# Kernel optimization log

Measured on AMD Instinct MI355X. Metric: run time of the kernel, lower is better.

The kernel has to match this reference:

```python
import jax, jax.numpy as jnp
import numpy as np

N, F, M, E = 8192, 256, 128, 131072


def setup_inputs() -> dict:
    key = jax.random.key(0)
    k = jax.random.split(key, 6)
    x = jax.random.normal(k[0], (N, F), dtype=jnp.float32)
    edge_index = jax.random.randint(k[1], (2, E), 0, N, dtype=jnp.int64)
    eps = jax.random.normal(k[2], (N, M), dtype=jnp.float32)
    # small init scale so sigmoid(z_i . z_j) isn't saturated
    W_mu = jax.random.normal(k[3], (F, M), dtype=jnp.float32) * 0.05
    b_mu = jnp.zeros((M,), dtype=jnp.float32)
    W_sig = jax.random.normal(k[4], (F, M), dtype=jnp.float32) * 0.05
    b_sig = jnp.zeros((M,), dtype=jnp.float32)
    return {"x": x, "edge_index": edge_index, "eps": eps,
            "W_mu": W_mu, "b_mu": b_mu, "W_sig": W_sig, "b_sig": b_sig}


def reference(x, edge_index, eps, W_mu, b_mu, W_sig, b_sig):
    # Gaussian encoder: Normal(mu, exp(logstd)), Independent over latent dim
    mu = x @ W_mu + b_mu                      # [N, M]
    logstd = x @ W_sig + b_sig                # [N, M]
    sigma = jnp.exp(logstd)
    z = mu + sigma * eps                      # rsample, [N, M]

    # decoder.probability(dot(z_i, z_j)) = sigmoid(logit); vectorized as Z @ Z.T
    logits = z @ z.T                          # [N, N]

    # symmetric adjacency labels from edge_index (either direction counts)
    src, dst = edge_index[0], edge_index[1]
    adj = jnp.zeros((N, N), dtype=jnp.float32)
    adj = adj.at[src, dst].set(1.0)
    adj = adj.at[dst, src].set(1.0)

    # BCE(sigmoid(s), y) summed over unordered pairs i < j (stable logits form)
    per_pair = jax.nn.softplus(logits) - adj * logits  # = -[y log p + (1-y) log(1-p)]
    triu = jnp.triu(jnp.ones((N, N), dtype=bool), k=1)
    bce = jnp.sum(jnp.where(triu, per_pair, 0.0))

    # sum_i KL( N(mu_i, sigma_i) || N(0, I) )
    kl = jnp.sum(0.5 * (sigma * sigma + mu * mu - 1.0) - logstd)

    return bce + 0.001 * kl
```

## Files before the change

kernel.cpp:

```cpp
#include <hip/hip_runtime.h>

#define NN 8192
#define FF 256
#define MM 128
#define HSLOTS 262144

typedef __attribute__((ext_vector_type(8))) short bf16x8;
typedef __attribute__((ext_vector_type(4))) float f32x4;

#define P_KL    0
#define P_EDGE  (64 * 16)
#define P_SP    (128 * 16)
#define Z_OFF   16384
#define Z_BYTES (NN * MM * 2)
#define HASH_OFF (Z_OFF + Z_BYTES)
#define WT_OFF  (HASH_OFF + HSLOTS * 4)
#define WT_BYTES (MM * FF * 2)

__device__ __forceinline__ float wave_reduce(float v) {
    #pragma unroll
    for (int off = 32; off > 0; off >>= 1) v += __shfl_down(v, off);
    return v;
}
__device__ __forceinline__ unsigned short f2bf(float f) {
    unsigned int u = __float_as_uint(f);
    u += 0x7fffu + ((u >> 16) & 1u);
    return (unsigned short)(u >> 16);
}
__device__ __forceinline__ int4 pack8(float4 a, float4 b) {
    int4 p;
    p.x = (int)f2bf(a.x) | ((int)f2bf(a.y) << 16);
    p.y = (int)f2bf(a.z) | ((int)f2bf(a.w) << 16);
    p.z = (int)f2bf(b.x) | ((int)f2bf(b.y) << 16);
    p.w = (int)f2bf(b.z) | ((int)f2bf(b.w) << 16);
    return p;
}

__global__ __launch_bounds__(256)
void prep_w(const float* __restrict__ Wmu, const float* __restrict__ Wsg,
            unsigned short* __restrict__ WmuT, unsigned short* __restrict__ WsgT,
            float* __restrict__ part, unsigned int* __restrict__ ht) {
    const int t = blockIdx.x * 256 + threadIdx.x;
    const int n = t >> 8, f = t & 255;
    WmuT[t] = f2bf(Wmu[f * MM + n]);
    WsgT[t] = f2bf(Wsg[f * MM + n]);
    if (t < 4096) part[t] = 0.f;
    uint4 z4 = {0u, 0u, 0u, 0u};
    ((uint4*)ht)[t * 2]     = z4;
    ((uint4*)ht)[t * 2 + 1] = z4;
}

#define XP_I4 33
#define XP_S  264

__global__ __launch_bounds__(256)
void encoder_mfma(const float* __restrict__ x, const float* __restrict__ eps,
                  const unsigned short* __restrict__ WmuT,
                  const unsigned short* __restrict__ WsgT,
                  const float* __restrict__ bmu, const float* __restrict__ bsg,
                  unsigned short* __restrict__ zb, float* __restrict__ part) {
    __shared__ int4 ax[16 * XP_I4];
    __shared__ float red[4];
    const int tid = threadIdx.x;
    const int wid = tid >> 6, lane = tid & 63;
    const int l15 = lane & 15, quad = lane >> 4;
    const int row0 = blockIdx.x * 16;

    {
        const int r = tid >> 4, ch = tid & 15;
        const float4* g0 = (const float4*)(x + (size_t)(row0 + r) * FF + ch * 8);
        const float4* g1 = (const float4*)(x + (size_t)(row0 + r) * FF + (ch + 16) * 8);
        ax[r * XP_I4 + ch]      = pack8(g0[0], g0[1]);
        ax[r * XP_I4 + ch + 16] = pack8(g1[0], g1[1]);
    }
    __syncthreads();

    const short* sax = (const short*)ax;
    const int4* wtm = (const int4*)WmuT;
    const int4* wts = (const int4*)WsgT;

    f32x4 zero4 = {0.f, 0.f, 0.f, 0.f};
    f32x4 accm[2], accl[2];
    accm[0] = accm[1] = accl[0] = accl[1] = zero4;

    #pragma unroll
    for (int ks = 0; ks < 8; ++ks) {
        const bf16x8 a = *(const bf16x8*)&sax[l15 * XP_S + ks * 32 + quad * 8];
        #pragma unroll
        for (int j = 0; j < 2; ++j) {
            const int n = wid * 32 + j * 16 + l15;
            const bf16x8 bmf = *(const bf16x8*)&wtm[n * 32 + ks * 4 + quad];
            const bf16x8 bsf = *(const bf16x8*)&wts[n * 32 + ks * 4 + quad];
            accm[j] = __builtin_amdgcn_mfma_f32_16x16x32_bf16(a, bmf, accm[j], 0, 0, 0);
            accl[j] = __builtin_amdgcn_mfma_f32_16x16x32_bf16(a, bsf, accl[j], 0, 0, 0);
        }
    }

    float klp = 0.f;
    #pragma unroll
    for (int j = 0; j < 2; ++j) {
        const int col = wid * 32 + j * 16 + l15;
        const float bm = bmu[col], bs = bsg[col];
        #pragma unroll
        for (int r = 0; r < 4; ++r) {
            const int row = row0 + quad * 4 + r;
            const float mu = accm[j][r] + bm;
            const float ls = accl[j][r] + bs;
            const float sg = __expf(ls);
            const float zz = fmaf(sg, eps[(size_t)row * MM + col], mu);
            zb[(size_t)row * MM + col] = f2bf(zz);
            klp += 0.5f * (sg * sg + mu * mu - 1.f) - ls;
        }
    }

    klp = wave_reduce(klp);
    if (lane == 0) red[wid] = klp;
    __syncthreads();
    if (tid == 0)
        atomicAdd(&part[P_KL + (blockIdx.x & 63) * 16],
                  red[0] + red[1] + red[2] + red[3]);
}

__device__ __forceinline__ float dotpair(unsigned int a, unsigned int b) {
    const float al = __uint_as_float(a << 16);
    const float ah = __uint_as_float(a & 0xffff0000u);
    const float bl = __uint_as_float(b << 16);
    const float bh = __uint_as_float(b & 0xffff0000u);
    return fmaf(al, bl, ah * bh);
}

__global__ __launch_bounds__(256)
void edge_kernel(const int* __restrict__ ei, int E,
                 const unsigned short* __restrict__ zb,
                 unsigned int* __restrict__ ht, float* __restrict__ part) {
    const int e = blockIdx.x * 256 + threadIdx.x;
    float contrib = 0.f;
    if (e < E) {
        const int i = ei[e];
        const int j = ei[E + e];
        if (i != j) {
            const int a = min(i, j), b = max(i, j);
            const unsigned int key = (unsigned int)a * NN + b;
            unsigned int slot = (key * 2654435761u) & (HSLOTS - 1);
            bool first = false;
            for (;;) {
                const unsigned int old = atomicCAS(&ht[slot], 0u, key);
                if (old == 0u) { first = true; break; }
                if (old == key) break;
                slot = (slot + 1) & (HSLOTS - 1);
            }
            if (first) {
                const uint4* za = (const uint4*)(zb + (size_t)a * MM);
                const uint4* zc = (const uint4*)(zb + (size_t)b * MM);
                float s = 0.f;
                #pragma unroll
                for (int q = 0; q < MM / 8; ++q) {
                    const uint4 ua = za[q], ub = zc[q];
                    s += dotpair(ua.x, ub.x) + dotpair(ua.y, ub.y)
                       + dotpair(ua.z, ub.z) + dotpair(ua.w, ub.w);
                }
                contrib = s;
            }
        }
    }
    contrib = wave_reduce(contrib);
    if ((threadIdx.x & 63) == 0)
        atomicAdd(&part[P_EDGE + (blockIdx.x & 63) * 16], contrib);
}

__global__ __launch_bounds__(256, 3)
void tile_kernel(const unsigned short* __restrict__ zb, float* __restrict__ part) {
    const int bi = blockIdx.y, bj = blockIdx.x;
    if (bj < bi) return;

    __shared__ int4 la[128 * 8];
    __shared__ int4 lb[128 * 8];

    const int tid = threadIdx.x;
    const int wid = tid >> 6, lane = tid & 63;
    const int wm = wid >> 1, wn = wid & 1;
    const int l15 = lane & 15, quad = lane >> 4;
    const int xk = l15 & 7;

    const int4* ga = (const int4*)(zb + (size_t)bi * 128 * MM);
    const int4* gb = (const int4*)(zb + (size_t)bj * 128 * MM);

    f32x4 zero4 = {0.f, 0.f, 0.f, 0.f};
    f32x4 acc[4][4];
    #pragma unroll
    for (int i = 0; i < 4; ++i)
        #pragma unroll
        for (int j = 0; j < 4; ++j) acc[i][j] = zero4;

    const short* sa = (const short*)la;
    const short* sb = (const short*)lb;

    #pragma unroll
    for (int kc = 0; kc < 2; ++kc) {
        if (kc) __syncthreads();
        #pragma unroll
        for (int i = 0; i < 4; ++i) {
            const int c = tid + i * 256;
            const int row = c >> 3, ch = c & 7;
            const int sl = ch ^ (row & 7);
            la[row * 8 + sl] = ga[row * 16 + kc * 8 + ch];
            lb[row * 8 + sl] = gb[row * 16 + kc * 8 + ch];
        }
        __syncthreads();
        #pragma unroll
        for (int ks = 0; ks < 2; ++ks) {
            const int kq = ks * 4 + quad;
            bf16x8 af[4], bfr[4];
            #pragma unroll
            for (int t = 0; t < 4; ++t) {
                const int ar = wm * 64 + t * 16 + l15;
                af[t]  = *(const bf16x8*)&sa[ar * 64 + ((kq ^ xk) * 8)];
                const int br = wn * 64 + t * 16 + l15;
                bfr[t] = *(const bf16x8*)&sb[br * 64 + ((kq ^ xk) * 8)];
            }
            #pragma unroll
            for (int i = 0; i < 4; ++i)
                #pragma unroll
                for (int j = 0; j < 4; ++j)
                    acc[i][j] = __builtin_amdgcn_mfma_f32_16x16x32_bf16(
                        af[i], bfr[j], acc[i][j], 0, 0, 0);
        }
    }

    float tsum = 0.f;
    if (bi != bj) {
        #pragma unroll
        for (int i = 0; i < 4; ++i)
            #pragma unroll
            for (int j = 0; j < 4; ++j)
                #pragma unroll
                for (int r = 0; r < 4; ++r) {
                    const float v = acc[i][j][r];
                    const float e = __expf(-fabsf(v));
                    tsum += fmaxf(v, 0.f) + e * fmaf(e, -0.5f, 1.f);
                }
    } else {
        const int rbase = wm * 64 + quad * 4;
        const int cbase = wn * 64 + l15;
        #pragma unroll
        for (int i = 0; i < 4; ++i)
            #pragma unroll
            for (int j = 0; j < 4; ++j)
                #pragma unroll
                for (int r = 0; r < 4; ++r)
                    if (cbase + j * 16 > rbase + i * 16 + r) {
                        const float v = acc[i][j][r];
                        const float e = __expf(-fabsf(v));
                        tsum += fmaxf(v, 0.f) + e * fmaf(e, -0.5f, 1.f);
                    }
    }

    tsum = wave_reduce(tsum);
    if (lane == 0)
        atomicAdd(&part[P_SP + ((bi * 64 + bj + wid * 16) & 63) * 16], tsum);
}

__global__ void combine_kernel(const float* __restrict__ part,
                               float* __restrict__ out) {
    const int t = threadIdx.x;
    float v = part[P_SP + t * 16] - part[P_EDGE + t * 16]
            + 0.001f * part[P_KL + t * 16];
    v = wave_reduce(v);
    if (t == 0) out[0] = v;
}

extern "C" void kernel_launch(void* const* d_in, const int* in_sizes, int n_in,
                              void* d_out, int out_size, void* d_ws, size_t ws_size,
                              hipStream_t stream) {
    const float* x   = (const float*)d_in[0];
    const int* ei    = (const int*)d_in[1];
    const float* eps = (const float*)d_in[2];
    const float* Wmu = (const float*)d_in[3];
    const float* bmu = (const float*)d_in[4];
    const float* Wsg = (const float*)d_in[5];
    const float* bsg = (const float*)d_in[6];
    float* out = (float*)d_out;
    char* ws = (char*)d_ws;

    float* part = (float*)ws;
    unsigned short* zb = (unsigned short*)(ws + Z_OFF);
    unsigned int* ht = (unsigned int*)(ws + HASH_OFF);
    unsigned short* WmuT = (unsigned short*)(ws + WT_OFF);
    unsigned short* WsgT = (unsigned short*)(ws + WT_OFF + WT_BYTES);
    const int E = in_sizes[1] / 2;

    prep_w<<<128, 256, 0, stream>>>(Wmu, Wsg, WmuT, WsgT, part, ht);
    encoder_mfma<<<NN / 16, 256, 0, stream>>>(x, eps, WmuT, WsgT, bmu, bsg, zb, part);
    edge_kernel<<<(E + 255) / 256, 256, 0, stream>>>(ei, E, zb, ht, part);
    dim3 grid(NN / 128, NN / 128);
    tile_kernel<<<grid, 256, 0, stream>>>(zb, part);
    combine_kernel<<<1, 64, 0, stream>>>(part, out);
}
```

Baseline: 129.6 us.

## Cooperative edge dot products, triangular tile grid, direct-global MFMA fragment loads

The edge kernel now has each group of 16 lanes compute one edge's 128-dim dot product cooperatively, using coalesced 16-byte loads and a shuffle reduction. Only the group leader does the hash dedup. The tile kernel launches only the 2080 upper-triangular blocks, mapping the linear index to (bi,bj) with a sqrt formula, so the half of the blocks that exited early no longer launch. It also drops LDS staging and loads MFMA fragments straight from global memory, relying on L2/L1 reuse instead of shared memory, and removes the occupancy hint from launch bounds. The cost is that some dot products are now computed for duplicate edges and then discarded, and the tile loads are now uncoalesced and rely on the cache.

```diff
diff --git a/kernel.cpp b/kernel.cpp
--- a/kernel.cpp
+++ b/kernel.cpp
@@ -133,13 +133,31 @@
 void edge_kernel(const int* __restrict__ ei, int E,
                  const unsigned short* __restrict__ zb,
                  unsigned int* __restrict__ ht, float* __restrict__ part) {
-    const int e = blockIdx.x * 256 + threadIdx.x;
-    float contrib = 0.f;
-    if (e < E) {
-        const int i = ei[e];
-        const int j = ei[E + e];
-        if (i != j) {
-            const int a = min(i, j), b = max(i, j);
+    const int tid = threadIdx.x;
+    const int wid = tid >> 6, lane = tid & 63;
+    const int g = lane >> 4, l15 = lane & 15;
+    const int base0 = blockIdx.x * 128 + wid * 32;
+
+    float accum = 0.f;
+    #pragma unroll 2
+    for (int p = 0; p < 8; ++p) {
+        const int e = base0 + p * 4 + g;
+        float s = 0.f;
+        int i = 0, j = 0, a = 0, b = 0;
+        if (e < E) {
+            i = ei[e];
+            j = ei[E + e];
+            a = min(i, j); b = max(i, j);
+            const uint4 ua = ((const uint4*)(zb + (size_t)a * MM))[l15];
+            const uint4 ub = ((const uint4*)(zb + (size_t)b * MM))[l15];
+            s = dotpair(ua.x, ub.x) + dotpair(ua.y, ub.y)
+              + dotpair(ua.z, ub.z) + dotpair(ua.w, ub.w);
+        }
+        s += __shfl_down(s, 8);
+        s += __shfl_down(s, 4);
+        s += __shfl_down(s, 2);
+        s += __shfl_down(s, 1);
+        if (l15 == 0 && e < E && i != j) {
             const unsigned int key = (unsigned int)a * NN + b;
             unsigned int slot = (key * 2654435761u) & (HSLOTS - 1);
             bool first = false;
@@ -149,41 +167,30 @@
                 if (old == key) break;
                 slot = (slot + 1) & (HSLOTS - 1);
             }
-            if (first) {
-                const uint4* za = (const uint4*)(zb + (size_t)a * MM);
-                const uint4* zc = (const uint4*)(zb + (size_t)b * MM);
-                float s = 0.f;
-                #pragma unroll
-                for (int q = 0; q < MM / 8; ++q) {
-                    const uint4 ua = za[q], ub = zc[q];
-                    s += dotpair(ua.x, ub.x) + dotpair(ua.y, ub.y)
-                       + dotpair(ua.z, ub.z) + dotpair(ua.w, ub.w);
-                }
-                contrib = s;
-            }
-        }
-    }
-    contrib = wave_reduce(contrib);
-    if ((threadIdx.x & 63) == 0)
-        atomicAdd(&part[P_EDGE + (blockIdx.x & 63) * 16], contrib);
-}
-
-__global__ __launch_bounds__(256, 3)
+            if (first) accum += s;
+        }
+    }
+    accum = wave_reduce(accum);
+    if (lane == 0)
+        atomicAdd(&part[P_EDGE + ((blockIdx.x * 4 + wid) & 63) * 16], accum);
+}
+
+__global__ __launch_bounds__(256)
 void tile_kernel(const unsigned short* __restrict__ zb, float* __restrict__ part) {
-    const int bi = blockIdx.y, bj = blockIdx.x;
-    if (bj < bi) return;
-
-    __shared__ int4 la[128 * 8];
-    __shared__ int4 lb[128 * 8];
+    const int q = blockIdx.x;
+    int bi = (int)((129.0f - sqrtf(fmaxf(129.0f * 129.0f - 8.0f * (float)q, 0.f))) * 0.5f);
+    bi = max(0, min(bi, 63));
+    while ((bi + 1) * (129 - (bi + 1)) / 2 <= q && bi < 63) ++bi;
+    while (bi * (129 - bi) / 2 > q) --bi;
+    const int bj = bi + (q - bi * (129 - bi) / 2);
 
     const int tid = threadIdx.x;
     const int wid = tid >> 6, lane = tid & 63;
     const int wm = wid >> 1, wn = wid & 1;
     const int l15 = lane & 15, quad = lane >> 4;
-    const int xk = l15 & 7;
-
-    const int4* ga = (const int4*)(zb + (size_t)bi * 128 * MM);
-    const int4* gb = (const int4*)(zb + (size_t)bj * 128 * MM);
+
+    const unsigned short* arow = zb + (size_t)(bi * 128 + wm * 64 + l15) * MM + quad * 8;
+    const unsigned short* brow = zb + (size_t)(bj * 128 + wn * 64 + l15) * MM + quad * 8;
 
     f32x4 zero4 = {0.f, 0.f, 0.f, 0.f};
     f32x4 acc[4][4];
@@ -192,39 +199,20 @@
         #pragma unroll
         for (int j = 0; j < 4; ++j) acc[i][j] = zero4;
 
-    const short* sa = (const short*)la;
-    const short* sb = (const short*)lb;
-
-    #pragma unroll
-    for (int kc = 0; kc < 2; ++kc) {
-        if (kc) __syncthreads();
-        #pragma unroll
-        for (int i = 0; i < 4; ++i) {
-            const int c = tid + i * 256;
-            const int row = c >> 3, ch = c & 7;
-            const int sl = ch ^ (row & 7);
-            la[row * 8 + sl] = ga[row * 16 + kc * 8 + ch];
-            lb[row * 8 + sl] = gb[row * 16 + kc * 8 + ch];
-        }
-        __syncthreads();
-        #pragma unroll
-        for (int ks = 0; ks < 2; ++ks) {
-            const int kq = ks * 4 + quad;
-            bf16x8 af[4], bfr[4];
+    #pragma unroll
+    for (int ks = 0; ks < 4; ++ks) {
+        bf16x8 af[4], bfr[4];
+        #pragma unroll
+        for (int t = 0; t < 4; ++t) {
+            af[t]  = *(const bf16x8*)(arow + t * 16 * MM + ks * 32);
+            bfr[t] = *(const bf16x8*)(brow + t * 16 * MM + ks * 32);
+        }
+        #pragma unroll
+        for (int i = 0; i < 4; ++i)
             #pragma unroll
-            for (int t = 0; t < 4; ++t) {
-                const int ar = wm * 64 + t * 16 + l15;
-                af[t]  = *(const bf16x8*)&sa[ar * 64 + ((kq ^ xk) * 8)];
-                const int br = wn * 64 + t * 16 + l15;
-                bfr[t] = *(const bf16x8*)&sb[br * 64 + ((kq ^ xk) * 8)];
-            }
-            #pragma unroll
-            for (int i = 0; i < 4; ++i)
-                #pragma unroll
-                for (int j = 0; j < 4; ++j)
-                    acc[i][j] = __builtin_amdgcn_mfma_f32_16x16x32_bf16(
-                        af[i], bfr[j], acc[i][j], 0, 0, 0);
-        }
+            for (int j = 0; j < 4; ++j)
+                acc[i][j] = __builtin_amdgcn_mfma_f32_16x16x32_bf16(
+                    af[i], bfr[j], acc[i][j], 0, 0, 0);
     }
 
     float tsum = 0.f;
@@ -257,7 +245,7 @@
 
     tsum = wave_reduce(tsum);
     if (lane == 0)
-        atomicAdd(&part[P_SP + ((bi * 64 + bj + wid * 16) & 63) * 16], tsum);
+        atomicAdd(&part[P_SP + ((q * 4 + wid) & 63) * 16], tsum);
 }
 
 __global__ void combine_kernel(const float* __restrict__ part,
@@ -291,8 +279,7 @@
 
     prep_w<<<128, 256, 0, stream>>>(Wmu, Wsg, WmuT, WsgT, part, ht);
     encoder_mfma<<<NN / 16, 256, 0, stream>>>(x, eps, WmuT, WsgT, bmu, bsg, zb, part);
-    edge_kernel<<<(E + 255) / 256, 256, 0, stream>>>(ei, E, zb, ht, part);
-    dim3 grid(NN / 128, NN / 128);
-    tile_kernel<<<grid, 256, 0, stream>>>(zb, part);
+    edge_kernel<<<(E + 127) / 128, 256, 0, stream>>>(ei, E, zb, ht, part);
+    tile_kernel<<<2080, 256, 0, stream>>>(zb, part);
     combine_kernel<<<1, 64, 0, stream>>>(part, out);
 }
```

Measured after the change: 152.4 us. 1.18x slower.
